# Performance work log

Measured on AMD Instinct MI355X. Metric: run time of the kernel, lower is better.

Reference implementation:

```python
import jax, jax.numpy as jnp
import numpy as np

B, S, D = 2, 2048, 2048
H, HKV = 16, 4
HD = D // H  # 128
ROPE_BASE = 10000.0


def _rope(t, cos, sin):
    # t: [B, h, S, HD]; torch variant: x1 = even dims, x2 = odd dims,
    # output = concat([x1*cos - x2*sin, x1*sin + x2*cos], axis=-1)
    x1 = t[..., ::2]
    x2 = t[..., 1::2]
    return jnp.concatenate([x1 * cos - x2 * sin, x1 * sin + x2 * cos], axis=-1)


def setup_inputs() -> dict:
    key = jax.random.key(0)
    kx, kq, kk, kv, ko = jax.random.split(key, 5)
    x = jax.random.normal(kx, (B, S, D), dtype=jnp.float32)
    scale = 0.02
    Wq = jax.random.normal(kq, (D, H * HD), dtype=jnp.float32) * scale
    Wk = jax.random.normal(kk, (D, HKV * HD), dtype=jnp.float32) * scale
    Wv = jax.random.normal(kv, (D, HKV * HD), dtype=jnp.float32) * scale
    Wo = jax.random.normal(ko, (H * HD, D), dtype=jnp.float32) * scale
    mask = jnp.tril(jnp.ones((S, S), dtype=bool))  # causal
    return {"x": x, "Wq": Wq, "Wk": Wk, "Wv": Wv, "Wo": Wo, "mask": mask}


def reference(x, Wq, Wk, Wv, Wo, mask):
    b, s, d = x.shape
    # projections: [B,S,h,HD] -> [B,h,S,HD]
    q = (x @ Wq).reshape(b, s, H, HD).transpose(0, 2, 1, 3)
    k = (x @ Wk).reshape(b, s, HKV, HD).transpose(0, 2, 1, 3)
    v = (x @ Wv).reshape(b, s, HKV, HD).transpose(0, 2, 1, 3)

    # RoPE tables: [S, HD/2]
    theta = 1.0 / (ROPE_BASE ** (jnp.arange(0, HD, 2, dtype=jnp.float32) / HD))
    angles = jnp.arange(s, dtype=jnp.float32)[:, None] * theta
    cos, sin = jnp.cos(angles), jnp.sin(angles)

    q = _rope(q, cos, sin)
    k = _rope(k, cos, sin)

    # GQA: repeat_interleave kv heads along head dim
    rep = H // HKV
    k = jnp.repeat(k, rep, axis=1)
    v = jnp.repeat(v, rep, axis=1)

    scores = jnp.einsum("bhqd,bhkd->bhqk", q, k) / jnp.sqrt(jnp.float32(HD))
    scores = jnp.where(mask, scores, -jnp.inf)
    attn = jax.nn.softmax(scores, axis=-1)

    out = jnp.einsum("bhqk,bhkd->bqhd", attn, v).reshape(b, s, H * HD)
    return out @ Wo
```

## Files before the change

kernel.cpp:

```cpp
#include <hip/hip_runtime.h>

typedef __bf16 bf16;
typedef __bf16 bf16x8 __attribute__((ext_vector_type(8)));
typedef float f32x4 __attribute__((ext_vector_type(4)));
typedef short s16x4 __attribute__((ext_vector_type(4)));

#define B_ 2
#define S_ 2048
#define D_ 2048
#define H_ 16
#define HKV_ 4
#define HD_ 128
#define QKVW 3072
#define QKW 2560
#define SCALE 0.08838834764831845f
#define NEGINF -30000.0f

__device__ inline void gload16(const void* g, void* l) {
  __builtin_amdgcn_global_load_lds((const __attribute__((address_space(1))) unsigned int*)g,
                                   (__attribute__((address_space(3))) unsigned int*)l, 16, 0, 0);
}

__device__ inline unsigned short bfb(float v) {
  union { bf16 h; unsigned short u; } c;
  c.h = (bf16)v;
  return c.u;
}

__global__ void detect_dtype(const unsigned* __restrict__ xw, int* __restrict__ flag) {
  __shared__ int cnt;
  if (threadIdx.x == 0) cnt = 0;
  __syncthreads();
  unsigned w = xw[(size_t)threadIdx.x * 16384];
  unsigned low = w & 0xFFFFu;
  int e = (int)((low >> 7) & 0xFF);
  int vote = (low == 0u || (e >= 100 && e <= 140)) ? 1 : 0;
  atomicAdd(&cnt, vote);
  __syncthreads();
  if (threadIdx.x == 0) *flag = (cnt >= 128) ? 1 : 0;
}

__global__ __launch_bounds__(256) void transpose_qkvw(
    const void* __restrict__ Wq, const void* __restrict__ Wk, const void* __restrict__ Wv,
    bf16* __restrict__ wqkvT, const int* __restrict__ flag) {
  int z = blockIdx.z;
  const void* in = (z == 0) ? Wq : (z == 1) ? Wk : Wv;
  int cols = (z == 0) ? 2048 : 512;
  bf16* out = wqkvT + ((z == 0) ? 0 : (z == 1) ? 2048 * 2048 : 2560 * 2048);
  if (blockIdx.x * 32 >= cols) return;
  int fm = *flag;
  __shared__ float tile[32][33];
  int c0 = blockIdx.x * 32, r0 = blockIdx.y * 32;
  int tx = threadIdx.x, ty = threadIdx.y;
#pragma unroll
  for (int i = 0; i < 32; i += 8) {
    long idx = (long)(r0 + ty + i) * cols + c0 + tx;
    tile[ty + i][tx] = fm ? (float)((const bf16*)in)[idx] : ((const float*)in)[idx];
  }
  __syncthreads();
#pragma unroll
  for (int i = 0; i < 32; i += 8)
    out[(long)(c0 + ty + i) * 2048 + r0 + tx] = (bf16)tile[tx][ty + i];
}

__global__ __launch_bounds__(256) void transpose_cvt(
    const void* __restrict__ in, bf16* __restrict__ out,
    long in_stride, long out_stride, const int* __restrict__ flag) {
  __shared__ float tile[32][33];
  int fm = *flag;
  int c0 = blockIdx.x * 32, r0 = blockIdx.y * 32;
  int tx = threadIdx.x, ty = threadIdx.y;
#pragma unroll
  for (int i = 0; i < 32; i += 8) {
    long idx = (long)(r0 + ty + i) * in_stride + c0 + tx;
    tile[ty + i][tx] = fm ? (float)((const bf16*)in)[idx] : ((const float*)in)[idx];
  }
  __syncthreads();
#pragma unroll
  for (int i = 0; i < 32; i += 8)
    out[(long)(c0 + ty + i) * out_stride + r0 + tx] = (bf16)tile[tx][ty + i];
}

#define BM 128
#define BN 128
#define BK 32

__global__ __launch_bounds__(256) void gemm_bt(
    const void* __restrict__ A, const bf16* __restrict__ Bt, void* __restrict__ C,
    int M, int N, int K, int ldc, int ncmax,
    bf16* __restrict__ vt_out, int vcol0,
    const int* __restrict__ flag, int adyn, int cdyn) {
  alignas(16) __shared__ bf16 la[2 * BM * BK];
  alignas(16) __shared__ bf16 lb[2 * BN * BK];
  int fm = flag ? *flag : 1;
  bool af32 = adyn && !fm;
  bool cf32 = cdyn && !fm;
  int tid = threadIdx.x;
  int wave = tid >> 6, lane = tid & 63;
  int wr = wave >> 1, wc = wave & 1;
  int quad = lane >> 4, l16 = lane & 15;

  int nwg = (int)(gridDim.x * gridDim.y);
  int flat = (int)(blockIdx.y * gridDim.x + blockIdx.x);
  int cpx = nwg >> 3;
  int wk = (flat & 7) * cpx + (flat >> 3);
  int bx = wk % (int)gridDim.x, by = wk / (int)gridDim.x;
  int m0 = by * BM, n0 = bx * BN;

  f32x4 acc[4][4] = {};

  int sr = (wave << 4) + (lane >> 2);
  int sc = (((lane & 3) - (sr >> 1)) & 3) << 3;
  const bf16* gb0 = Bt + (long)(n0 + sr) * K + sc;
  const bf16* gb1 = Bt + (long)(n0 + 64 + sr) * K + sc;
  int lo0 = (wave << 9);
  int lo1 = 2048 + (wave << 9);
  const bf16* ga0 = nullptr; const bf16* ga1 = nullptr;
  const float* gaf = nullptr;
  int fr = tid >> 1, fh = (tid & 1) << 4;
  if (af32) gaf = (const float*)A + (long)(m0 + fr) * K + fh;
  else { ga0 = (const bf16*)A + (long)(m0 + sr) * K + sc;
         ga1 = (const bf16*)A + (long)(m0 + 64 + sr) * K + sc; }
  int c0 = fh >> 3;
  int k2 = (fr >> 1) & 3;
  int ws0 = ((c0 + k2) & 3) << 3;
  int ws1 = ((c0 + 1 + k2) & 3) << 3;

  int nk = K / BK;

  auto cvtwrite = [&](const float4* f, int buf) {
    alignas(16) bf16 tt[16];
#pragma unroll
    for (int u = 0; u < 4; u++) {
      tt[4 * u] = (bf16)f[u].x; tt[4 * u + 1] = (bf16)f[u].y;
      tt[4 * u + 2] = (bf16)f[u].z; tt[4 * u + 3] = (bf16)f[u].w;
    }
    bf16* rowp = la + (buf << 12) + fr * BK;
    *(uint4*)(rowp + ws0) = *(uint4*)tt;
    *(uint4*)(rowp + ws1) = *(uint4*)(tt + 8);
  };
  auto compute = [&](int buf) {
    const bf16* baA = la + (buf << 12);
    const bf16* baB = lb + (buf << 12);
    bf16x8 afr[4], bfr[4];
#pragma unroll
    for (int i = 0; i < 4; i++) {
      int rowA = (wr << 6) + (i << 4) + l16;
      afr[i] = *(const bf16x8*)(baA + rowA * BK + (((quad + (rowA >> 1)) & 3) << 3));
    }
#pragma unroll
    for (int j = 0; j < 4; j++) {
      int rowB = (wc << 6) + (j << 4) + l16;
      bfr[j] = *(const bf16x8*)(baB + rowB * BK + (((quad + (rowB >> 1)) & 3) << 3));
    }
#pragma unroll
    for (int i = 0; i < 4; i++)
#pragma unroll
      for (int j = 0; j < 4; j++)
        acc[i][j] = __builtin_amdgcn_mfma_f32_16x16x32_bf16(afr[i], bfr[j], acc[i][j], 0, 0, 0);
  };

  gload16(gb0, lb + lo0);
  gload16(gb1, lb + lo1);
  if (af32) {
    float4 f0[4];
#pragma unroll
    for (int u = 0; u < 4; u++) f0[u] = *(const float4*)(gaf + 4 * u);
    cvtwrite(f0, 0);
  } else {
    gload16(ga0, la + lo0);
    gload16(ga1, la + lo1);
  }
  __syncthreads();

  for (int t = 0; t < nk; ++t) {
    int cur = t & 1, nxt = cur ^ 1;
    bool hasnext = (t + 1 < nk);
    float4 f[4];
    if (hasnext) {
      int k0 = (t + 1) * BK;
      gload16(gb0 + k0, lb + (nxt << 12) + lo0);
      gload16(gb1 + k0, lb + (nxt << 12) + lo1);
      if (af32) {
        const float* fp = gaf + k0;
#pragma unroll
        for (int u = 0; u < 4; u++) f[u] = *(const float4*)(fp + 4 * u);
      } else {
        gload16(ga0 + k0, la + (nxt << 12) + lo0);
        gload16(ga1 + k0, la + (nxt << 12) + lo1);
      }
    }

    compute(cur);

    if (hasnext && af32) cvtwrite(f, nxt);
    __syncthreads();
  }

  if (vt_out && n0 >= vcol0) {
#pragma unroll
    for (int i = 0; i < 4; i++)
#pragma unroll
      for (int j = 0; j < 4; j++) {
        int col = n0 + (wc << 6) + (j << 4) + l16;
        int hdg = col - vcol0;
        int row0 = m0 + (wr << 6) + (i << 4) + (quad << 2);
        int bb = row0 >> 11, s = row0 & 2047;
        ushort4 p;
        p.x = bfb(acc[i][j][0]); p.y = bfb(acc[i][j][1]);
        p.z = bfb(acc[i][j][2]); p.w = bfb(acc[i][j][3]);
        *(ushort4*)(vt_out + (((long)(bb * 512 + hdg)) << 11) + s) = p;
      }
  } else {
#pragma unroll
    for (int i = 0; i < 4; i++)
#pragma unroll
      for (int j = 0; j < 4; j++) {
        int col = n0 + (wc << 6) + (j << 4) + l16;
        if (col >= ncmax) continue;
#pragma unroll
        for (int r = 0; r < 4; r++) {
          long row = m0 + (wr << 6) + (i << 4) + (quad << 2) + r;
          float v = acc[i][j][r];
          if (cf32) ((float*)C)[row * ldc + col] = v;
          else      ((bf16*)C)[row * ldc + col] = (bf16)v;
        }
      }
  }
}

__global__ __launch_bounds__(256) void rope_scatter(
    const bf16* __restrict__ qkv, bf16* __restrict__ Q, bf16* __restrict__ Ko) {
  int row = blockIdx.x;
  int b = row >> 11, s = row & 2047;
  int tid = threadIdx.x;
  int i = tid & 63;
  const bf16* src = qkv + (long)row * QKW;
  float theta = __expf(-0.14391156831212787f * (float)i);
  float sn, cs;
  sincosf((float)s * theta, &sn, &cs);
#pragma unroll
  for (int it = 0; it < 4; ++it) {
    int h = (tid + it * 256) >> 6;
    unsigned v = *(const unsigned*)(src + h * 128 + 2 * i);
    float x1 = __uint_as_float(v << 16);
    float x2 = __uint_as_float(v & 0xFFFF0000u);
    long qb = ((long)(b * H_ + h) * S_ + s) * HD_;
    Q[qb + i]      = (bf16)((x1 * cs - x2 * sn) * SCALE);
    Q[qb + 64 + i] = (bf16)((x1 * sn + x2 * cs) * SCALE);
  }
  {
    int kh = tid >> 6;
    unsigned v = *(const unsigned*)(src + 2048 + kh * 128 + 2 * i);
    float x1 = __uint_as_float(v << 16);
    float x2 = __uint_as_float(v & 0xFFFF0000u);
    long kb = ((long)(b * HKV_ + kh) * S_ + s) * HD_;
    Ko[kb + i]      = (bf16)(x1 * cs - x2 * sn);
    Ko[kb + 64 + i] = (bf16)(x1 * sn + x2 * cs);
  }
}

#define KTILE 8192
#define VTILE 8192

__global__ __launch_bounds__(256) void attn_kernel(
    const bf16* __restrict__ Q, const bf16* __restrict__ K,
    const bf16* __restrict__ Vt, bf16* __restrict__ O) {
  alignas(16) __shared__ bf16 Ks[2 * KTILE];
  alignas(16) __shared__ bf16 Vs[2 * VTILE];
  int bi = (int)blockIdx.x;
  int cb = bi & 7;
  int b = cb >> 2, kh = cb & 3;
  int r = bi >> 3;
  int qt0 = r >> 2;
  int h = kh * 4 + (r & 3);
  int tid = threadIdx.x, wave = tid >> 6, lane = tid & 63;
  int quad = lane >> 4, l16 = lane & 15;
  const bf16* Kg = K + ((long)(b * HKV_ + kh) * S_) * HD_;
  const bf16* Vg = Vt + ((long)(b * HKV_ + kh) * HD_) * S_;

  int kgo[4], vgo[4], klo[4], vlo[4];
#pragma unroll
  for (int u = 0; u < 4; u++) {
    int i = u * 4 + wave;
    int rr = i * 4 + quad;
    int c = l16 ^ (rr & 15);
    kgo[u] = rr * HD_ + c * 8;
    klo[u] = i * 512;
    int v = i * 8 + (lane >> 3);
    int cv = (lane & 7) ^ (v & 7);
    vgo[u] = v * S_ + cv * 8;
    vlo[u] = i * 512;
  }

  for (int hf = 0; hf < 2; ++hf) {
    int qt = hf ? 31 - qt0 : qt0;
    int q0 = qt * 64;
    const bf16* Qg = Q + ((long)(b * H_ + h) * S_ + q0) * HD_;

    bf16x8 qb[4];
    {
      const bf16* qrow = Qg + (wave * 16 + l16) * HD_ + quad * 8;
#pragma unroll
      for (int kk = 0; kk < 4; kk++) qb[kk] = *(const bf16x8*)(qrow + kk * 32);
    }

    if (hf) __syncthreads();

#pragma unroll
    for (int u = 0; u < 4; u++) {
      gload16(Kg + kgo[u], Ks + klo[u]);
      gload16(Vg + vgo[u], Vs + vlo[u]);
    }

    f32x4 Of[8] = {};
    float m_run = NEGINF, l_run = 0.f;

    for (int kt = 0; kt <= qt; ++kt) {
      __syncthreads();
      int p = kt & 1;
      if (kt < qt) {
        const bf16* kn = Kg + (long)(kt + 1) * 8192;
        const bf16* vn = Vg + (long)(kt + 1) * 64;
        bf16* kd = Ks + (p ^ 1) * KTILE;
        bf16* vd = Vs + (p ^ 1) * VTILE;
#pragma unroll
        for (int u = 0; u < 4; u++) {
          gload16(kn + kgo[u], kd + klo[u]);
          gload16(vn + vgo[u], vd + vlo[u]);
        }
      }
      const bf16* kc = Ks + p * KTILE;
      const bf16* vc = Vs + p * VTILE;

      bool diag = (kt == qt);
      f32x4 sf[4];
      __builtin_amdgcn_s_setprio(1);
#pragma unroll
      for (int jb = 0; jb < 4; jb++) {
        if (diag && jb > wave) {
          sf[jb] = (f32x4){NEGINF, NEGINF, NEGINF, NEGINF};
        } else {
          f32x4 a = {};
          const bf16* kbase = kc + (jb * 16 + l16) * 128;
#pragma unroll
          for (int kk = 0; kk < 4; kk++) {
            bf16x8 kf = *(const bf16x8*)(kbase + (((kk * 4 + quad) ^ l16) * 8));
            a = __builtin_amdgcn_mfma_f32_16x16x32_bf16(kf, qb[kk], a, 0, 0, 0);
          }
          sf[jb] = a;
        }
      }
      __builtin_amdgcn_s_setprio(0);
      if (diag) {
#pragma unroll
        for (int jb = 0; jb < 4; jb++)
          if (jb == wave) {
#pragma unroll
            for (int r2 = 0; r2 < 4; r2++)
              if (quad * 4 + r2 > l16) sf[jb][r2] = NEGINF;
          }
      }

      float mx = NEGINF;
#pragma unroll
      for (int jb = 0; jb < 4; jb++)
#pragma unroll
        for (int r2 = 0; r2 < 4; r2++) mx = fmaxf(mx, sf[jb][r2]);
      mx = fmaxf(mx, __shfl_xor(mx, 16));
      mx = fmaxf(mx, __shfl_xor(mx, 32));
      if (__any(mx > m_run + 8.0f)) {
        float mnew = fmaxf(m_run, mx);
        float alpha = __expf(m_run - mnew);
        m_run = mnew;
        l_run *= alpha;
#pragma unroll
        for (int n = 0; n < 8; n++) Of[n] *= alpha;
      }

      float ls = 0.f;
      s16x4 pk[4];
#pragma unroll
      for (int jb = 0; jb < 4; jb++) {
        float p0 = __expf(sf[jb][0] - m_run);
        float p1 = __expf(sf[jb][1] - m_run);
        float p2 = __expf(sf[jb][2] - m_run);
        float p3 = __expf(sf[jb][3] - m_run);
        ls += (p0 + p1) + (p2 + p3);
        s16x4 t;
        t.x = (short)bfb(p0); t.y = (short)bfb(p1);
        t.z = (short)bfb(p2); t.w = (short)bfb(p3);
        pk[jb] = t;
      }
      l_run += ls;

      __builtin_amdgcn_s_setprio(1);
#pragma unroll
      for (int jb = 0; jb < 4; jb++) {
        if (diag && jb > wave) continue;
#pragma unroll
        for (int n = 0; n < 8; n++) {
          int v = n * 16 + l16;
          const bf16* va_p = vc + v * 64 + (((jb * 2 + (quad >> 1)) ^ (l16 & 7)) * 8) + (quad & 1) * 4;
          s16x4 va = *(const s16x4*)va_p;
          Of[n] = __builtin_amdgcn_mfma_f32_16x16x16bf16_1k(va, pk[jb], Of[n], 0, 0, 0);
        }
      }
      __builtin_amdgcn_s_setprio(0);
    }

    l_run += __shfl_xor(l_run, 16);
    l_run += __shfl_xor(l_run, 32);
    float inv = 1.0f / fmaxf(l_run, 1e-30f);
    bf16* Ob = O + ((long)(b * S_) + q0 + wave * 16 + l16) * D_ + h * HD_;
#pragma unroll
    for (int n = 0; n < 8; n++) {
      ushort4 w;
      w.x = bfb(Of[n][0] * inv); w.y = bfb(Of[n][1] * inv);
      w.z = bfb(Of[n][2] * inv); w.w = bfb(Of[n][3] * inv);
      *(ushort4*)(Ob + n * 16 + quad * 4) = w;
    }
  }
}

extern "C" void kernel_launch(void* const* d_in, const int* in_sizes, int n_in,
                              void* d_out, int out_size, void* d_ws, size_t ws_size,
                              hipStream_t stream) {
  const void* x  = d_in[0];
  const void* Wq = d_in[1];
  const void* Wk = d_in[2];
  const void* Wv = d_in[3];
  const void* Wo = d_in[4];
  bf16* ws = (bf16*)d_ws;
  int* flag = (int*)d_ws;

  bf16* qkv   = ws + 16;
  bf16* Vtb   = ws + 10485776;
  bf16* Qb    = ws + 12582928;
  bf16* wqkvT = ws + 12582928;
  bf16* Kb    = ws + 20971536;
  bf16* attno = ws + 16;
  bf16* woT   = ws + 10485776;

  dim3 tb(32, 8);
  detect_dtype<<<1, 256, 0, stream>>>((const unsigned*)x, flag);
  transpose_qkvw<<<dim3(64, 64, 3), tb, 0, stream>>>(Wq, Wk, Wv, wqkvT, flag);
  gemm_bt<<<dim3(QKVW / BN, (B_ * S_) / BM), 256, 0, stream>>>(
      x, wqkvT, qkv, B_ * S_, QKVW, D_, QKW, QKW, Vtb, QKW, flag, 1, 0);
  rope_scatter<<<B_ * S_, 256, 0, stream>>>(qkv, Qb, Kb);
  attn_kernel<<<dim3(512, 1, 1), 256, 0, stream>>>(Qb, Kb, Vtb, attno);
  transpose_cvt<<<dim3(64, 64, 1), tb, 0, stream>>>(Wo, woT, 2048, 2048, flag);
  gemm_bt<<<dim3(D_ / BN, (B_ * S_) / BM), 256, 0, stream>>>(
      attno, woT, d_out, B_ * S_, D_, D_, D_, D_, nullptr, 0, flag, 0, 1);
}
```

Baseline: 383.0 us.

## Add wide 128x256 tile GEMM with XCD-aware block swizzle for QKV projection

Introduces a new 512-thread GEMM kernel with a 128x256 output tile, double-buffered LDS with swizzled layout, and a block index remap that groups workgroups across XCDs for L2 locality. The QKV projection now uses this kernel in place of the generic gemm_bt. The aim is more reuse of operand tiles per load and better cache sharing. In exchange it uses more LDS and registers per workgroup, which may lower occupancy, and it launches fewer workgroups.

```diff
diff --git a/kernel.cpp b/kernel.cpp
--- a/kernel.cpp
+++ b/kernel.cpp
@@ -229,6 +229,148 @@
   }
 }
 
+#define WBM 128
+#define WBN 256
+#define WBK 32
+
+__global__ __launch_bounds__(512, 4) void gemm_bt_wide(
+    const void* __restrict__ A, const bf16* __restrict__ Bt, bf16* __restrict__ C,
+    int K, int ldc, int ncmax,
+    bf16* __restrict__ vt_out, int vcol0, const int* __restrict__ flag) {
+  alignas(16) __shared__ bf16 la[2 * WBM * WBK];
+  alignas(16) __shared__ bf16 lb[2 * WBN * WBK];
+  int fm = flag ? *flag : 1;
+  bool af32 = !fm;
+  int tid = threadIdx.x;
+  int wave = tid >> 6, lane = tid & 63;
+  int wm = wave >> 2, wn = wave & 3;
+  int quad = lane >> 4, l16 = lane & 15;
+
+  int nwg = (int)(gridDim.x * gridDim.y);
+  int flat = (int)(blockIdx.y * gridDim.x + blockIdx.x);
+  int cpx = nwg >> 3;
+  int wk = (flat & 7) * cpx + (flat >> 3);
+  int bx = wk % (int)gridDim.x, by = wk / (int)gridDim.x;
+  int m0 = by * WBM, n0 = bx * WBN;
+
+  f32x4 acc[4][4] = {};
+
+  const bf16* gb[2];
+  int lbo[2];
+#pragma unroll
+  for (int u = 0; u < 2; u++) {
+    int sr2 = (wave << 5) + (u << 4) + (lane >> 2);
+    int sc2 = (((lane & 3) - (sr2 >> 1)) & 3) << 3;
+    gb[u] = Bt + (long)(n0 + sr2) * K + sc2;
+    lbo[u] = ((wave << 5) + (u << 4)) << 5;
+  }
+  const bf16* gaB = nullptr;
+  const float* gaf = nullptr;
+  int lao = (wave << 4) << 5;
+  int fr = tid >> 2, fc = tid & 3;
+  int wso = 0;
+  if (af32) {
+    gaf = (const float*)A + (long)(m0 + fr) * K + (fc << 3);
+    wso = (fr << 5) + ((((fc) + (fr >> 1)) & 3) << 3);
+  } else {
+    int ra = (wave << 4) + (lane >> 2);
+    int sca = (((lane & 3) - (ra >> 1)) & 3) << 3;
+    gaB = (const bf16*)A + (long)(m0 + ra) * K + sca;
+  }
+
+  int nk = K / WBK;
+
+  auto cvtwrite = [&](const float4* f, int buf) {
+    alignas(16) bf16 tt[8];
+    tt[0] = (bf16)f[0].x; tt[1] = (bf16)f[0].y; tt[2] = (bf16)f[0].z; tt[3] = (bf16)f[0].w;
+    tt[4] = (bf16)f[1].x; tt[5] = (bf16)f[1].y; tt[6] = (bf16)f[1].z; tt[7] = (bf16)f[1].w;
+    *(uint4*)(la + (buf << 12) + wso) = *(uint4*)tt;
+  };
+  auto compute = [&](int buf) {
+    const bf16* baA = la + (buf << 12);
+    const bf16* baB = lb + (buf << 13);
+    bf16x8 afr[4], bfr[4];
+#pragma unroll
+    for (int i = 0; i < 4; i++) {
+      int rowA = (wm << 6) + (i << 4) + l16;
+      afr[i] = *(const bf16x8*)(baA + (rowA << 5) + (((quad + (rowA >> 1)) & 3) << 3));
+    }
+#pragma unroll
+    for (int j = 0; j < 4; j++) {
+      int rowB = (wn << 6) + (j << 4) + l16;
+      bfr[j] = *(const bf16x8*)(baB + (rowB << 5) + (((quad + (rowB >> 1)) & 3) << 3));
+    }
+#pragma unroll
+    for (int i = 0; i < 4; i++)
+#pragma unroll
+      for (int j = 0; j < 4; j++)
+        acc[i][j] = __builtin_amdgcn_mfma_f32_16x16x32_bf16(afr[i], bfr[j], acc[i][j], 0, 0, 0);
+  };
+
+  gload16(gb[0], lb + lbo[0]);
+  gload16(gb[1], lb + lbo[1]);
+  if (af32) {
+    float4 f0[2];
+    f0[0] = *(const float4*)gaf;
+    f0[1] = *(const float4*)(gaf + 4);
+    cvtwrite(f0, 0);
+  } else {
+    gload16(gaB, la + lao);
+  }
+  __syncthreads();
+
+  for (int t = 0; t < nk; ++t) {
+    int cur = t & 1, nxt = cur ^ 1;
+    bool hasnext = (t + 1 < nk);
+    float4 f[2];
+    if (hasnext) {
+      int k0 = (t + 1) * WBK;
+      gload16(gb[0] + k0, lb + (nxt << 13) + lbo[0]);
+      gload16(gb[1] + k0, lb + (nxt << 13) + lbo[1]);
+      if (af32) {
+        f[0] = *(const float4*)(gaf + k0);
+        f[1] = *(const float4*)(gaf + k0 + 4);
+      } else {
+        gload16(gaB + k0, la + (nxt << 12) + lao);
+      }
+    }
+
+    compute(cur);
+
+    if (hasnext && af32) cvtwrite(f, nxt);
+    __syncthreads();
+  }
+
+  if (vt_out && n0 >= vcol0) {
+#pragma unroll
+    for (int i = 0; i < 4; i++)
+#pragma unroll
+      for (int j = 0; j < 4; j++) {
+        int col = n0 + (wn << 6) + (j << 4) + l16;
+        int hdg = col - vcol0;
+        int row0 = m0 + (wm << 6) + (i << 4) + (quad << 2);
+        int bb = row0 >> 11, s = row0 & 2047;
+        ushort4 p;
+        p.x = bfb(acc[i][j][0]); p.y = bfb(acc[i][j][1]);
+        p.z = bfb(acc[i][j][2]); p.w = bfb(acc[i][j][3]);
+        *(ushort4*)(vt_out + (((long)(bb * 512 + hdg)) << 11) + s) = p;
+      }
+  } else {
+#pragma unroll
+    for (int i = 0; i < 4; i++)
+#pragma unroll
+      for (int j = 0; j < 4; j++) {
+        int col = n0 + (wn << 6) + (j << 4) + l16;
+        if (col >= ncmax) continue;
+#pragma unroll
+        for (int r = 0; r < 4; r++) {
+          long row = m0 + (wm << 6) + (i << 4) + (quad << 2) + r;
+          C[row * ldc + col] = (bf16)acc[i][j][r];
+        }
+      }
+  }
+}
+
 __global__ __launch_bounds__(256) void rope_scatter(
     const bf16* __restrict__ qkv, bf16* __restrict__ Q, bf16* __restrict__ Ko) {
   int row = blockIdx.x;
@@ -445,8 +587,8 @@
   dim3 tb(32, 8);
   detect_dtype<<<1, 256, 0, stream>>>((const unsigned*)x, flag);
   transpose_qkvw<<<dim3(64, 64, 3), tb, 0, stream>>>(Wq, Wk, Wv, wqkvT, flag);
-  gemm_bt<<<dim3(QKVW / BN, (B_ * S_) / BM), 256, 0, stream>>>(
-      x, wqkvT, qkv, B_ * S_, QKVW, D_, QKW, QKW, Vtb, QKW, flag, 1, 0);
+  gemm_bt_wide<<<dim3(QKVW / WBN, (B_ * S_) / WBM), 512, 0, stream>>>(
+      x, wqkvT, qkv, D_, QKW, QKW, Vtb, QKW, flag);
   rope_scatter<<<B_ * S_, 256, 0, stream>>>(qkv, Qb, Kb);
   attn_kernel<<<dim3(512, 1, 1), 256, 0, stream>>>(Qb, Kb, Vtb, attno);
   transpose_cvt<<<dim3(64, 64, 1), tb, 0, stream>>>(Wo, woT, 2048, 2048, flag);
```

Result: no change. 380.0 us (-0.8%).
